# Optimization experiments

Hardware: AMD Instinct MI355X
Metric: run time of the kernel (lower is better)

## Reference

```python
import jax, jax.numpy as jnp
import numpy as np

BATCH = 2048
SEQ_LEN = 8192


def setup_inputs() -> dict:
    key = jax.random.key(0)
    k1, k2 = jax.random.split(key)
    inputs = jax.random.normal(k1, (BATCH, SEQ_LEN), dtype=jnp.float32)
    filters = jax.random.normal(k2, (BATCH, SEQ_LEN), dtype=jnp.float32)
    return {"inputs": inputs, "filters": filters}


def reference(inputs, filters):
    # FFT-based long convolution with zero-padding to 2L (linear, not circular, conv).
    # torch norm='forward': rfft divides by n, irfft multiplies by n -> net scale 1/n.
    L = inputs.shape[-1]
    n = 2 * L  # rfft with n=2L implicitly zero-pads, same as F.pad then rfft
    x_f = jnp.fft.rfft(inputs, n=n, axis=-1, norm="forward")   # (B, L+1) complex
    h_f = jnp.fft.rfft(filters, n=n, axis=-1, norm="forward")  # (B, L+1) complex
    y = jnp.fft.irfft(x_f * h_f, n=n, axis=-1, norm="forward")  # (B, 2L)
    return y[..., :L]
```

## Files before the change

### kernel.cpp

```cpp
#include <hip/hip_runtime.h>

#define L_LEN 8192
#define N_FFT 16384
#define NB    1024

#define LB __launch_bounds__(NB)

typedef float f2 __attribute__((ext_vector_type(2)));

__device__ __forceinline__ f2 mkf2(float a, float b) { f2 v; v.x = a; v.y = b; return v; }

__device__ __forceinline__ f2 cmul(f2 a, f2 w) {
    return mkf2(a.y, a.y) * mkf2(-w.y, w.x) + mkf2(a.x, a.x) * w;
}

__device__ __forceinline__ void sincos_rev(float rev, float* sn, float* cs) {
    *sn = __builtin_amdgcn_sinf(rev);
    *cs = __builtin_amdgcn_cosf(rev);
}
__device__ __forceinline__ f2 cis_rev(float rev) {
    return mkf2(__builtin_amdgcn_cosf(rev), __builtin_amdgcn_sinf(rev));
}

__host__ __device__ constexpr int swz(int i) {
    return i ^ ((((i) >> 4) ^ ((i) >> 8) ^ ((i) >> 12)) & 15);
}

__device__ __forceinline__ int rev6(int m) {
    int r = 0;
#pragma unroll
    for (int d = 0; d < 6; ++d) { r = (r << 2) | (m & 3); m >>= 2; }
    return r;
}

__device__ __forceinline__ void bfly_dif(f2& x0, f2& x1, f2& x2, f2& x3,
                                         f2 w1, f2 w2, f2 w3) {
    f2 A = x0 + x2, B = x0 - x2, C = x1 + x3, D = x1 - x3;
    f2 iD = mkf2(-D.y, D.x);
    x0 = A + C;
    x1 = cmul(B - iD, w1);
    x2 = cmul(A - C, w2);
    x3 = cmul(B + iD, w3);
}

__device__ __forceinline__ void bfly_dit(f2& x0, f2& x1, f2& x2, f2& x3,
                                         f2 w1, f2 w2, f2 w3) {
    f2 a1 = cmul(x1, w1), a2 = cmul(x2, w2), a3 = cmul(x3, w3);
    f2 E = x0 + a2, F = x0 - a2, G = a1 + a3, K = a1 - a3;
    f2 iK = mkf2(-K.y, K.x);
    x0 = E + G; x1 = F + iK; x2 = E - G; x3 = F - iK;
}

__device__ __forceinline__ void bfly_dif1(f2* z) {
    f2 A = z[0] + z[2], B = z[0] - z[2], C = z[1] + z[3], D = z[1] - z[3];
    f2 iD = mkf2(-D.y, D.x);
    z[0] = A + C; z[1] = B - iD; z[2] = A - C; z[3] = B + iD;
}

__device__ __forceinline__ f2 pwY(f2 Zm, f2 Zr) {
    f2 half = mkf2(0.5f, 0.5f);
    f2 X = half * (Zm + mkf2(Zr.x, -Zr.y));
    f2 H = half * (mkf2(Zm.y, -Zm.x) + mkf2(Zr.y, Zr.x));
    return cmul(X, H);
}

#define CT0 1.0f
#define CT1 0.92387953251128674f
#define CT2 0.70710678118654752f
#define CT3 0.38268343236508977f
#define ST1 0.38268343236508977f
#define ST2 0.70710678118654752f
#define ST3 0.92387953251128674f

__device__ __forceinline__ void fwd_first(f2* lds, int tid,
                                          const float* __restrict__ xr,
                                          const float* __restrict__ hr) {
    f2 r[4][4];
    float snA, csA;
    sincos_rev((float)tid * (-1.0f / 16384.f), &snA, &csA);
    f2 u1 = mkf2(csA, snA);
    const f2 lad[4] = {mkf2(CT0, 0.f), mkf2(CT1, -ST1), mkf2(CT2, -ST2), mkf2(CT3, -ST3)};
#pragma unroll
    for (int jB = 0; jB < 4; ++jB) {
        const int t = tid + jB * 1024;
        f2 z0 = mkf2(xr[t], hr[t]);
        f2 z1 = mkf2(xr[t + 4096], hr[t + 4096]);
        f2 w1 = (jB == 0) ? u1 : cmul(u1, lad[jB]);
        f2 w2 = cmul(w1, w1);
        f2 w3 = cmul(w2, w1);
        f2 iz1 = mkf2(-z1.y, z1.x);
        r[0][jB] = z0 + z1;
        r[1][jB] = cmul(z0 - iz1, w1);
        r[2][jB] = cmul(z0 - z1, w2);
        r[3][jB] = cmul(z0 + iz1, w3);
    }
    float sn, cs;
    sincos_rev((float)tid * (-1.0f / 4096.f), &sn, &cs);
    f2 v1 = mkf2(cs, sn);
    f2 v2 = cmul(v1, v1);
    f2 v3 = cmul(v2, v1);
#pragma unroll
    for (int jA = 0; jA < 4; ++jA)
        bfly_dif(r[jA][0], r[jA][1], r[jA][2], r[jA][3], v1, v2, v3);

    const int sb = swz(tid);
#pragma unroll
    for (int jA = 0; jA < 4; ++jA)
#pragma unroll
        for (int jB = 0; jB < 4; ++jB)
            lds[sb ^ swz(jA * 4096 + jB * 1024)] = r[jA][jB];
}

template<int QA>
__device__ __forceinline__ void fwd_pair(f2* lds, int tid) {
    constexpr int QB = QA / 4;
    const int g = tid / QB;
    const int u = tid % QB;
    const int sb = swz(g * (4 * QA) + u);
    f2 r[4][4];
#pragma unroll
    for (int jA = 0; jA < 4; ++jA)
#pragma unroll
        for (int jB = 0; jB < 4; ++jB)
            r[jA][jB] = lds[sb ^ swz(jA * QA + jB * QB)];

    {
        float sn, cs;
        sincos_rev((float)u * (-1.0f / (float)(4 * QA)), &sn, &cs);
        f2 u1 = mkf2(cs, sn);
        const f2 lad[4] = {mkf2(CT0, 0.f), mkf2(CT1, -ST1), mkf2(CT2, -ST2), mkf2(CT3, -ST3)};
#pragma unroll
        for (int jB = 0; jB < 4; ++jB) {
            f2 w1 = (jB == 0) ? u1 : cmul(u1, lad[jB]);
            f2 w2 = cmul(w1, w1);
            f2 w3 = cmul(w2, w1);
            bfly_dif(r[0][jB], r[1][jB], r[2][jB], r[3][jB], w1, w2, w3);
        }
    }
    {
        float sn, cs;
        sincos_rev((float)u * (-1.0f / (float)(4 * QB)), &sn, &cs);
        f2 v1 = mkf2(cs, sn);
        f2 v2 = cmul(v1, v1);
        f2 v3 = cmul(v2, v1);
#pragma unroll
        for (int jA = 0; jA < 4; ++jA)
            bfly_dif(r[jA][0], r[jA][1], r[jA][2], r[jA][3], v1, v2, v3);
    }

#pragma unroll
    for (int jA = 0; jA < 4; ++jA)
#pragma unroll
        for (int jB = 0; jB < 4; ++jB)
            lds[sb ^ swz(jA * QA + jB * QB)] = r[jA][jB];
}

__device__ __forceinline__ void combo_item(const f2* lds, int b, f2* Zi, int* sl) {
    const int sA = swz(4 * rev6(b));
    const int sB = swz(4 * rev6(4096 - b));
    f2 A[4], B[4];
#pragma unroll
    for (int k = 0; k < 4; ++k) { A[k] = lds[sA ^ k]; B[k] = lds[sB ^ k]; }
    bfly_dif1(A);
    bfly_dif1(B);
    f2 Yb   = pwY(A[0], B[3]);
    f2 Yb4  = pwY(A[1], B[2]);
    f2 Yb8  = pwY(A[2], B[1]);
    f2 Yb12 = pwY(A[3], B[0]);
    f2 t = cis_rev((float)b * (1.0f / 16384.f));
    f2 S  = Yb + Yb8,   D  = Yb - Yb8;
    f2 Sp = Yb4 + Yb12, Dp = Yb4 - Yb12;
    f2 c  = cmul(D, t);
    f2 cp = cmul(Dp, t);
    Zi[0] = mkf2(S.x - c.y,    S.y + c.x);
    Zi[1] = Sp - cp;
    Zi[2] = mkf2(Sp.x + cp.x, -(Sp.y + cp.y));
    Zi[3] = mkf2(S.x + c.y,   -S.y + c.x);
    const int sbase = (b & 1) ? 4097 : 0;
    const int ra = rev6(b >> 1);
    const int rc = rev6((4096 - b) >> 1);
    sl[0] = sbase ^ swz(ra);
    sl[1] = sl[0] ^ 2;
    sl[2] = sbase ^ swz(rc);
    sl[3] = sl[2] ^ 2;
}

__device__ __forceinline__ void combo_special(const f2* lds, f2* Zi, int* sl) {
    f2 z[4];
#pragma unroll
    for (int k = 0; k < 4; ++k) z[k] = lds[k];
    bfly_dif1(z);
    float Y0 = z[0].x * z[0].y;
    float Y8 = z[2].x * z[2].y;
    f2 Y4096 = pwY(z[1], z[3]);
    Zi[0] = mkf2(Y0 + Y8, Y0 - Y8);          sl[0] = 0;
    Zi[1] = mkf2(2.f * Y4096.x, -2.f * Y4096.y); sl[1] = 2;
    f2 w[4];
#pragma unroll
    for (int k = 0; k < 4; ++k) w[k] = lds[8 + k];
    bfly_dif1(w);
    f2 Y2048 = pwY(w[0], w[3]);
    f2 Y6144 = pwY(w[1], w[2]);
    f2 cj6 = mkf2(Y6144.x, -Y6144.y);
    f2 S1 = Y2048 + cj6, D1 = Y2048 - cj6;
    f2 t1 = mkf2(0.70710678118654752f, 0.70710678118654752f);
    f2 c1 = cmul(D1, t1);
    Zi[2] = mkf2(S1.x - c1.y, S1.y + c1.x);  sl[2] = 1;
    f2 cj2 = mkf2(Y2048.x, -Y2048.y);
    f2 S2 = Y6144 + cj2, D2 = Y6144 - cj2;
    f2 t2 = mkf2(-0.70710678118654752f, 0.70710678118654752f);
    f2 c2 = cmul(D2, t2);
    Zi[3] = mkf2(S2.x - c2.y, S2.y + c2.x);  sl[3] = 3;
}

template<int QA>
__device__ __forceinline__ void inv_half(f2* lds, int th) {
    constexpr int QB = 4 * QA;
    const int h = th >> 8;
    const int k = th & 255;
    const int g = k / QA, u = k % QA;
    const int base = g * (16 * QA) + u;
    const int sb = (h ? 4097 : 0) ^ swz(base);
    f2 r[4][4];
#pragma unroll
    for (int jA = 0; jA < 4; ++jA)
#pragma unroll
        for (int jB = 0; jB < 4; ++jB)
            r[jA][jB] = lds[sb ^ swz(jA * QA + jB * QB)];

    {
        f2 a1;
        if constexpr (QA == 1) a1 = mkf2(1.f, 0.f);
        else { float sn, cs; sincos_rev((float)u * (1.0f / (float)(4 * QA)), &sn, &cs); a1 = mkf2(cs, sn); }
        f2 a2 = cmul(a1, a1), a3 = cmul(a2, a1);
#pragma unroll
        for (int jB = 0; jB < 4; ++jB)
            bfly_dit(r[0][jB], r[1][jB], r[2][jB], r[3][jB], a1, a2, a3);
    }
    {
        f2 b1;
        if constexpr (QA == 1) b1 = mkf2(1.f, 0.f);
        else { float sn, cs; sincos_rev((float)u * (1.0f / (float)(16 * QA)), &sn, &cs); b1 = mkf2(cs, sn); }
        const f2 lad[4] = {mkf2(CT0, 0.f), mkf2(CT1, ST1), mkf2(CT2, ST2), mkf2(CT3, ST3)};
#pragma unroll
        for (int jA = 0; jA < 4; ++jA) {
            f2 w1 = (jA == 0) ? b1 : cmul(b1, lad[jA]);
            f2 w2 = cmul(w1, w1), w3 = cmul(w2, w1);
            bfly_dit(r[jA][0], r[jA][1], r[jA][2], r[jA][3], w1, w2, w3);
        }
    }
#pragma unroll
    for (int jA = 0; jA < 4; ++jA)
#pragma unroll
        for (int jB = 0; jB < 4; ++jB)
            lds[sb ^ swz(jA * QA + jB * QB)] = r[jA][jB];
}

__device__ __forceinline__ void inv_last(const f2* lds, int tid,
                                         float* __restrict__ orow) {
    const float sc = 1.0f / (16384.f * 16384.f);
#pragma unroll
    for (int i = 0; i < 4; ++i) {
        const int m = tid + i * 1024;
        const int sm = swz(m);
        f2 P = lds[sm];
        f2 Q = lds[sm ^ 4097];
        f2 t = cis_rev((float)m * (1.0f / 8192.f));
        f2 w = P + cmul(Q, t);
        *(f2*)(orow + 2 * m) = mkf2(w.x * sc, w.y * sc);
    }
}

__global__ LB
void fftconv_kernel(const float* __restrict__ xin,
                    const float* __restrict__ hin,
                    float* __restrict__ out)
{
    __shared__ f2 lds[N_FFT];

    const int row = blockIdx.x;
    const int tid = threadIdx.x;
    const float* xr = xin + (size_t)row * L_LEN;
    const float* hr = hin + (size_t)row * L_LEN;

    fwd_first(lds, tid, xr, hr);
    __syncthreads();
    fwd_pair<256>(lds, tid);
    asm volatile("" ::: "memory");
    fwd_pair<16>(lds, tid);
    __syncthreads();

    {
        f2 Zi0[4], Zi1[4];
        int s0[4], s1[4];
        if (tid == 0) combo_special(lds, Zi0, s0);
        else          combo_item(lds, tid, Zi0, s0);
        combo_item(lds, tid + 1024, Zi1, s1);
        __syncthreads();
#pragma unroll
        for (int k = 0; k < 4; ++k) { lds[s0[k]] = Zi0[k]; lds[s1[k]] = Zi1[k]; }
    }
    __syncthreads();

    if (tid < 512) {
        inv_half<1>(lds, tid);
        asm volatile("" ::: "memory");
        inv_half<16>(lds, tid);
    }
    __syncthreads();
    if (tid < 512) inv_half<256>(lds, tid);
    __syncthreads();

    inv_last(lds, tid, out + (size_t)row * L_LEN);
}

extern "C" void kernel_launch(void* const* d_in, const int* in_sizes, int n_in,
                              void* d_out, int out_size, void* d_ws, size_t ws_size,
                              hipStream_t stream) {
    const float* x = (const float*)d_in[0];
    const float* h = (const float*)d_in[1];
    float* out = (float*)d_out;
    const int rows = in_sizes[0] / L_LEN;
    fftconv_kernel<<<dim3(rows), dim3(NB), 0, stream>>>(x, h, out);
}
```

Baseline: 107.5 us.

## Store FFT intermediates in LDS as packed fp16 with rescaling

```diff
diff --git a/kernel.cpp b/kernel.cpp
--- a/kernel.cpp
+++ b/kernel.cpp
@@ -1,4 +1,5 @@
 #include <hip/hip_runtime.h>
+#include <hip/hip_fp16.h>
 
 #define L_LEN 8192
 #define N_FFT 16384
@@ -14,6 +15,16 @@
     return mkf2(a.y, a.y) * mkf2(-w.y, w.x) + mkf2(a.x, a.x) * w;
 }
 
+__device__ __forceinline__ unsigned pk16(f2 v) {
+    __half2 h = __float22half2_rn(make_float2(v.x, v.y));
+    unsigned u; __builtin_memcpy(&u, &h, 4); return u;
+}
+__device__ __forceinline__ f2 up16(unsigned u) {
+    __half2 h; __builtin_memcpy(&h, &u, 4);
+    float2 f = __half22float2(h);
+    return mkf2(f.x, f.y);
+}
+
 __device__ __forceinline__ void sincos_rev(float rev, float* sn, float* cs) {
     *sn = __builtin_amdgcn_sinf(rev);
     *cs = __builtin_amdgcn_cosf(rev);
@@ -23,7 +34,7 @@
 }
 
 __host__ __device__ constexpr int swz(int i) {
-    return i ^ ((((i) >> 4) ^ ((i) >> 8) ^ ((i) >> 12)) & 15);
+    return i ^ ((((i) >> 5) ^ ((i) >> 10)) & 31);
 }
 
 __device__ __forceinline__ int rev6(int m) {
@@ -58,9 +69,9 @@
 }
 
 __device__ __forceinline__ f2 pwY(f2 Zm, f2 Zr) {
-    f2 half = mkf2(0.5f, 0.5f);
-    f2 X = half * (Zm + mkf2(Zr.x, -Zr.y));
-    f2 H = half * (mkf2(Zm.y, -Zm.x) + mkf2(Zr.y, Zr.x));
+    f2 q = mkf2(0.125f, 0.125f);
+    f2 X = q * (Zm + mkf2(Zr.x, -Zr.y));
+    f2 H = q * (mkf2(Zm.y, -Zm.x) + mkf2(Zr.y, Zr.x));
     return cmul(X, H);
 }
 
@@ -72,7 +83,7 @@
 #define ST2 0.70710678118654752f
 #define ST3 0.92387953251128674f
 
-__device__ __forceinline__ void fwd_first(f2* lds, int tid,
+__device__ __forceinline__ void fwd_first(unsigned* lds, int tid,
                                           const float* __restrict__ xr,
                                           const float* __restrict__ hr) {
     f2 r[4][4];
@@ -108,11 +119,11 @@
     for (int jA = 0; jA < 4; ++jA)
 #pragma unroll
         for (int jB = 0; jB < 4; ++jB)
-            lds[sb ^ swz(jA * 4096 + jB * 1024)] = r[jA][jB];
+            lds[sb ^ swz(jA * 4096 + jB * 1024)] = pk16(r[jA][jB]);
 }
 
 template<int QA>
-__device__ __forceinline__ void fwd_pair(f2* lds, int tid) {
+__device__ __forceinline__ void fwd_pair(unsigned* lds, int tid) {
     constexpr int QB = QA / 4;
     const int g = tid / QB;
     const int u = tid % QB;
@@ -122,7 +133,7 @@
     for (int jA = 0; jA < 4; ++jA)
 #pragma unroll
         for (int jB = 0; jB < 4; ++jB)
-            r[jA][jB] = lds[sb ^ swz(jA * QA + jB * QB)];
+            r[jA][jB] = up16(lds[sb ^ swz(jA * QA + jB * QB)]);
 
     {
         float sn, cs;
@@ -152,15 +163,15 @@
     for (int jA = 0; jA < 4; ++jA)
 #pragma unroll
         for (int jB = 0; jB < 4; ++jB)
-            lds[sb ^ swz(jA * QA + jB * QB)] = r[jA][jB];
-}
-
-__device__ __forceinline__ void combo_item(const f2* lds, int b, f2* Zi, int* sl) {
+            lds[sb ^ swz(jA * QA + jB * QB)] = pk16(r[jA][jB]);
+}
+
+__device__ __forceinline__ void combo_item(const unsigned* lds, int b, f2* Zi, int* sl) {
     const int sA = swz(4 * rev6(b));
     const int sB = swz(4 * rev6(4096 - b));
     f2 A[4], B[4];
 #pragma unroll
-    for (int k = 0; k < 4; ++k) { A[k] = lds[sA ^ k]; B[k] = lds[sB ^ k]; }
+    for (int k = 0; k < 4; ++k) { A[k] = up16(lds[sA ^ k]); B[k] = up16(lds[sB ^ k]); }
     bfly_dif1(A);
     bfly_dif1(B);
     f2 Yb   = pwY(A[0], B[3]);
@@ -176,7 +187,7 @@
     Zi[1] = Sp - cp;
     Zi[2] = mkf2(Sp.x + cp.x, -(Sp.y + cp.y));
     Zi[3] = mkf2(S.x + c.y,   -S.y + c.x);
-    const int sbase = (b & 1) ? 4097 : 0;
+    const int sbase = (b & 1) ? swz(4096) : 0;
     const int ra = rev6(b >> 1);
     const int rc = rev6((4096 - b) >> 1);
     sl[0] = sbase ^ swz(ra);
@@ -185,19 +196,19 @@
     sl[3] = sl[2] ^ 2;
 }
 
-__device__ __forceinline__ void combo_special(const f2* lds, f2* Zi, int* sl) {
+__device__ __forceinline__ void combo_special(const unsigned* lds, f2* Zi, int* sl) {
     f2 z[4];
 #pragma unroll
-    for (int k = 0; k < 4; ++k) z[k] = lds[k];
+    for (int k = 0; k < 4; ++k) z[k] = up16(lds[k]);
     bfly_dif1(z);
-    float Y0 = z[0].x * z[0].y;
-    float Y8 = z[2].x * z[2].y;
+    float Y0 = 0.0625f * z[0].x * z[0].y;
+    float Y8 = 0.0625f * z[2].x * z[2].y;
     f2 Y4096 = pwY(z[1], z[3]);
-    Zi[0] = mkf2(Y0 + Y8, Y0 - Y8);          sl[0] = 0;
+    Zi[0] = mkf2(Y0 + Y8, Y0 - Y8);              sl[0] = 0;
     Zi[1] = mkf2(2.f * Y4096.x, -2.f * Y4096.y); sl[1] = 2;
     f2 w[4];
 #pragma unroll
-    for (int k = 0; k < 4; ++k) w[k] = lds[8 + k];
+    for (int k = 0; k < 4; ++k) w[k] = up16(lds[8 + k]);
     bfly_dif1(w);
     f2 Y2048 = pwY(w[0], w[3]);
     f2 Y6144 = pwY(w[1], w[2]);
@@ -214,19 +225,19 @@
 }
 
 template<int QA>
-__device__ __forceinline__ void inv_half(f2* lds, int th) {
+__device__ __forceinline__ void inv_half(unsigned* lds, int th) {
     constexpr int QB = 4 * QA;
     const int h = th >> 8;
     const int k = th & 255;
     const int g = k / QA, u = k % QA;
     const int base = g * (16 * QA) + u;
-    const int sb = (h ? 4097 : 0) ^ swz(base);
+    const int sb = (h ? swz(4096) : 0) ^ swz(base);
     f2 r[4][4];
 #pragma unroll
     for (int jA = 0; jA < 4; ++jA)
 #pragma unroll
         for (int jB = 0; jB < 4; ++jB)
-            r[jA][jB] = lds[sb ^ swz(jA * QA + jB * QB)];
+            r[jA][jB] = up16(lds[sb ^ swz(jA * QA + jB * QB)]);
 
     {
         f2 a1;
@@ -249,22 +260,24 @@
             bfly_dit(r[jA][0], r[jA][1], r[jA][2], r[jA][3], w1, w2, w3);
         }
     }
-#pragma unroll
-    for (int jA = 0; jA < 4; ++jA)
-#pragma unroll
-        for (int jB = 0; jB < 4; ++jB)
-            lds[sb ^ swz(jA * QA + jB * QB)] = r[jA][jB];
-}
-
-__device__ __forceinline__ void inv_last(const f2* lds, int tid,
+    const f2 s = mkf2(0.0625f, 0.0625f);
+#pragma unroll
+    for (int jA = 0; jA < 4; ++jA)
+#pragma unroll
+        for (int jB = 0; jB < 4; ++jB)
+            lds[sb ^ swz(jA * QA + jB * QB)] = pk16(r[jA][jB] * s);
+}
+
+__device__ __forceinline__ void inv_last(const unsigned* lds, int tid,
                                          float* __restrict__ orow) {
-    const float sc = 1.0f / (16384.f * 16384.f);
+    const float sc = 1.0f / 4096.f;
+    const int s4096 = swz(4096);
 #pragma unroll
     for (int i = 0; i < 4; ++i) {
         const int m = tid + i * 1024;
         const int sm = swz(m);
-        f2 P = lds[sm];
-        f2 Q = lds[sm ^ 4097];
+        f2 P = up16(lds[sm]);
+        f2 Q = up16(lds[sm ^ s4096]);
         f2 t = cis_rev((float)m * (1.0f / 8192.f));
         f2 w = P + cmul(Q, t);
         *(f2*)(orow + 2 * m) = mkf2(w.x * sc, w.y * sc);
@@ -276,7 +289,7 @@
                     const float* __restrict__ hin,
                     float* __restrict__ out)
 {
-    __shared__ f2 lds[N_FFT];
+    __shared__ unsigned lds[N_FFT];
 
     const int row = blockIdx.x;
     const int tid = threadIdx.x;
@@ -298,7 +311,7 @@
         combo_item(lds, tid + 1024, Zi1, s1);
         __syncthreads();
 #pragma unroll
-        for (int k = 0; k < 4; ++k) { lds[s0[k]] = Zi0[k]; lds[s1[k]] = Zi1[k]; }
+        for (int k = 0; k < 4; ++k) { lds[s0[k]] = pk16(Zi0[k]); lds[s1[k]] = pk16(Zi1[k]); }
     }
     __syncthreads();
 
```

Result: slower. 116.6 us (+8.5%).
